# Optimization experiments

Hardware: AMD Instinct MI355X
Metric: run time of the kernel (lower is better)

Reference implementation:

```python
import jax, jax.numpy as jnp
import numpy as np

N, E, D, L, G = 100000, 800000, 64, 5, 256
ATOM_VOCAB, BOND_VOCAB = 119, 5
BN_EPS = 1e-5

def _bn(h, g, b):
    # BatchNorm1d in training mode: batch mean / biased var over nodes
    m = h.mean(0)
    v = h.var(0)
    return g * (h - m) * jax.lax.rsqrt(v + BN_EPS) + b

def setup_inputs() -> dict:
    key = jax.random.key(0)
    ks = jax.random.split(key, 12)
    xavier = lambda k, fi, fo: jax.random.uniform(k, (fi, fo), jnp.float32,
                                                  -np.sqrt(6.0/(fi+fo)), np.sqrt(6.0/(fi+fo)))
    return {
        "batch": jnp.sort(jax.random.randint(ks[0], (N,), 0, G)),
        "x": jax.random.randint(ks[1], (N, 1), 0, ATOM_VOCAB),
        "edge_index": jax.random.randint(ks[2], (2, E), 0, N),
        "edge_attr": jax.random.randint(ks[3], (E, 1), 0, BOND_VOCAB),
        "atom_emb": jax.random.normal(ks[4], (ATOM_VOCAB, D), jnp.float32),
        "bond_emb": jax.random.normal(ks[5], (BOND_VOCAB, D), jnp.float32),
        "W1": jnp.stack([xavier(jax.random.fold_in(ks[6], i), D, 2*D) for i in range(L)]),
        "b1": jnp.zeros((L, 2*D), jnp.float32),
        "g1": jnp.ones((L, 2*D), jnp.float32),
        "be1": jnp.zeros((L, 2*D), jnp.float32),
        "W2": jnp.stack([xavier(jax.random.fold_in(ks[7], i), 2*D, D) for i in range(L)]),
        "b2": jnp.zeros((L, D), jnp.float32),
        "gbn": jnp.ones((L, D), jnp.float32),
        "bbn": jnp.zeros((L, D), jnp.float32),
    }

def reference(batch, x, edge_index, edge_attr, atom_emb, bond_emb,
              W1, b1, g1, be1, W2, b2, gbn, bbn):
    h = atom_emb[x[:, 0]]              # [N, D]
    ea = bond_emb[edge_attr[:, 0]]     # [E, D]
    src, dst = edge_index[0], edge_index[1]
    for i in range(L):
        msg = jax.nn.relu(h[src] + ea)                         # [E, D]
        aggr = jax.ops.segment_sum(msg, dst, num_segments=N)   # [N, D]
        z = h + aggr                                           # (1+eps)*x_i + aggr, eps=0
        z = _bn(z @ W1[i] + b1[i], g1[i], be1[i])
        z = jax.nn.relu(z) @ W2[i] + b2[i]
        h = _bn(z, gbn[i], bbn[i])                             # outer BN
        if i < L - 1:
            h = jax.nn.relu(h)                                 # drop_ratio = 0 -> no dropout
    xpool = jax.ops.segment_sum(h, batch, num_segments=G)      # global_add_pool
    return (xpool, h)
```

## Files before the change

kernel.cpp:

```cpp
#include <hip/hip_runtime.h>
#include <cstdint>
#include <cstddef>

#define NN 100000
#define NP 100032
#define NE 800000
#define NG 256
#define NL 5
#define EPS 1e-5f
#define NSTRIPE 32

typedef __bf16 bf16x8 __attribute__((ext_vector_type(8)));
typedef float f32x4 __attribute__((ext_vector_type(4)));

__device__ __forceinline__ float bf2f(unsigned short u) {
  union { unsigned int i; float f; } x; x.i = ((unsigned int)u) << 16; return x.f;
}
__device__ __forceinline__ unsigned short f2bf(float f) {
  union { float f; unsigned int i; } x; x.f = f;
  unsigned int r = x.i + 0x7fffu + ((x.i >> 16) & 1u);
  return (unsigned short)(r >> 16);
}

__global__ __launch_bounds__(256) void prep_k(const int* __restrict__ x,
                                              const float* __restrict__ atom_emb,
                                              unsigned short* __restrict__ A,
                                              const float* __restrict__ W1,
                                              const float* __restrict__ W2,
                                              unsigned short* __restrict__ Wt1,
                                              unsigned short* __restrict__ Wt2,
                                              int* __restrict__ cnt) {
  int b = blockIdx.x, t = threadIdx.x;
  if (b < 3125) {
    int i = b * 256 + t;
    int n = i >> 3, c0 = (i & 7) * 8;
    const float* p = atom_emb + (size_t)x[n] * 64 + c0;
    float4 v0 = *(const float4*)p;
    float4 v1 = *(const float4*)(p + 4);
    union { bf16x8 b8; unsigned short u[8]; } o;
    o.u[0] = f2bf(v0.x); o.u[1] = f2bf(v0.y); o.u[2] = f2bf(v0.z); o.u[3] = f2bf(v0.w);
    o.u[4] = f2bf(v1.x); o.u[5] = f2bf(v1.y); o.u[6] = f2bf(v1.z); o.u[7] = f2bf(v1.w);
    *(bf16x8*)(A + (size_t)n * 64 + c0) = o.b8;
  } else if (b < 3445) {
    int i = (b - 3125) * 256 + t;
    const int S = NL * 128 * 64;
    if (i < S) {
      int l = i / (128 * 64), r = i % (128 * 64);
      int c = r / 64, k = r % 64;
      Wt1[i] = f2bf(W1[(size_t)l * 64 * 128 + (size_t)k * 128 + c]);
    } else {
      int j = i - S;
      int l = j / (128 * 64), r = j % (128 * 64);
      int c = r / 128, k = r % 128;
      Wt2[j] = f2bf(W2[(size_t)l * 128 * 64 + (size_t)k * 64 + c]);
    }
  } else {
    int i = (b - 3445) * 256 + t;
    if (i < NN) cnt[i] = 0;
  }
}

__global__ __launch_bounds__(256) void hist_k(const int* __restrict__ ei,
                                              int* __restrict__ cnt) {
  int e = blockIdx.x * 256 + threadIdx.x;
  if (e >= NE) return;
  atomicAdd(&cnt[ei[NE + e]], 1);
}

__global__ __launch_bounds__(256) void scan1_k(const int* __restrict__ cnt,
                                               int* __restrict__ rs,
                                               int* __restrict__ bsum) {
  __shared__ int sh[256];
  int t = threadIdx.x;
  int base = blockIdx.x * 1024 + t * 4;
  int v0 = 0, v1 = 0, v2 = 0, v3 = 0;
  if (base + 0 < NN) v0 = cnt[base + 0];
  if (base + 1 < NN) v1 = cnt[base + 1];
  if (base + 2 < NN) v2 = cnt[base + 2];
  if (base + 3 < NN) v3 = cnt[base + 3];
  int tsum = v0 + v1 + v2 + v3;
  sh[t] = tsum;
  __syncthreads();
  for (int off = 1; off < 256; off <<= 1) {
    int x = (t >= off) ? sh[t - off] : 0;
    __syncthreads();
    sh[t] += x;
    __syncthreads();
  }
  int excl = sh[t] - tsum;
  if (base + 0 < NN) rs[base + 0] = excl;
  if (base + 1 < NN) rs[base + 1] = excl + v0;
  if (base + 2 < NN) rs[base + 2] = excl + v0 + v1;
  if (base + 3 < NN) rs[base + 3] = excl + v0 + v1 + v2;
  if (t == 255) bsum[blockIdx.x] = sh[255];
}

__global__ __launch_bounds__(256) void scan3_k(int* __restrict__ rs,
                                               const int* __restrict__ bsum,
                                               int* __restrict__ cursor) {
  int i = blockIdx.x * 256 + threadIdx.x;
  int chunk = blockIdx.x >> 2;
  int boff = 0;
  for (int j = 0; j < chunk; ++j) boff += bsum[j];
  if (i < NN) {
    int v = rs[i] + boff;
    rs[i] = v;
    cursor[i] = v;
  }
  if (i == 0) rs[NN] = NE;
}

__global__ __launch_bounds__(256) void scatter_k(const int* __restrict__ ei,
                                                 const int* __restrict__ eattr,
                                                 int* __restrict__ cursor,
                                                 int* __restrict__ epack) {
  int band = blockIdx.x & 7;
  int e = (blockIdx.x >> 3) * 256 + threadIdx.x;
  if (e >= NE) return;
  int d = ei[NE + e];
  if (d / 12500 != band) return;
  int slot = atomicAdd(&cursor[d], 1);
  epack[slot] = (ei[e] << 3) | eattr[e];
}

template <int MODE>
__global__ __launch_bounds__(256) void csr_aggr_k(const int* __restrict__ rowstart,
                                                  const int* __restrict__ epack,
                                                  const float* __restrict__ bond,
                                                  const unsigned short* __restrict__ A,
                                                  const float* __restrict__ stat2prev,
                                                  const float* __restrict__ g,
                                                  const float* __restrict__ be,
                                                  unsigned short* __restrict__ B) {
  __shared__ float bl[5][68];
  __shared__ float scl64[64], shf64[64];
  int tid = threadIdx.x;
  for (int j = tid; j < 320; j += 256) bl[j >> 6][j & 63] = bond[j];
  if (MODE && tid < 64) {
    float s = 0.f, s2 = 0.f;
#pragma unroll
    for (int r = 0; r < NSTRIPE; ++r) {
      s += stat2prev[r * 128 + tid];
      s2 += stat2prev[r * 128 + 64 + tid];
    }
    float mean = s * (1.f / NN);
    float var = fmaxf(s2 * (1.f / NN) - mean * mean, 0.f);
    float sc = g[tid] * rsqrtf(var + EPS);
    scl64[tid] = sc;
    shf64[tid] = be[tid] - mean * sc;
  }
  __syncthreads();

  int lane = tid & 63;
  int sg = lane >> 3, ch = lane & 7, c0 = ch * 8;
  int row = blockIdx.x * 32 + (tid >> 6) * 8 + sg;
  float sc[8], sf[8];
  if (MODE) {
#pragma unroll
    for (int j = 0; j < 8; ++j) { sc[j] = scl64[c0 + j]; sf[j] = shf64[c0 + j]; }
  }
  int s = rowstart[row], e = rowstart[row + 1];
  float acc[8];
#pragma unroll
  for (int j = 0; j < 8; ++j) acc[j] = 0.f;
  int i = s;
  for (; i + 2 <= e; i += 2) {
    int p0 = epack[i], p1 = epack[i + 1];
    union { bf16x8 b; unsigned short u[8]; } h0, h1;
    h0.b = *(const bf16x8*)(A + (size_t)(p0 >> 3) * 64 + c0);
    h1.b = *(const bf16x8*)(A + (size_t)(p1 >> 3) * 64 + c0);
    const float* bp0 = &bl[p0 & 7][c0];
    const float* bp1 = &bl[p1 & 7][c0];
    float4 a0 = *(const float4*)(bp0), a1 = *(const float4*)(bp0 + 4);
    float4 d0 = *(const float4*)(bp1), d1 = *(const float4*)(bp1 + 4);
    float bb0[8] = {a0.x, a0.y, a0.z, a0.w, a1.x, a1.y, a1.z, a1.w};
    float bb1[8] = {d0.x, d0.y, d0.z, d0.w, d1.x, d1.y, d1.z, d1.w};
#pragma unroll
    for (int j = 0; j < 8; ++j) {
      float v0 = bf2f(h0.u[j]);
      float v1 = bf2f(h1.u[j]);
      if (MODE) {
        v0 = fmaxf(fmaf(v0, sc[j], sf[j]), 0.f);
        v1 = fmaxf(fmaf(v1, sc[j], sf[j]), 0.f);
      }
      acc[j] += fmaxf(v0 + bb0[j], 0.f);
      acc[j] += fmaxf(v1 + bb1[j], 0.f);
    }
  }
  if (i < e) {
    int p0 = epack[i];
    union { bf16x8 b; unsigned short u[8]; } h0;
    h0.b = *(const bf16x8*)(A + (size_t)(p0 >> 3) * 64 + c0);
    const float* bp0 = &bl[p0 & 7][c0];
    float4 a0 = *(const float4*)(bp0), a1 = *(const float4*)(bp0 + 4);
    float bb0[8] = {a0.x, a0.y, a0.z, a0.w, a1.x, a1.y, a1.z, a1.w};
#pragma unroll
    for (int j = 0; j < 8; ++j) {
      float v0 = bf2f(h0.u[j]);
      if (MODE) v0 = fmaxf(fmaf(v0, sc[j], sf[j]), 0.f);
      acc[j] += fmaxf(v0 + bb0[j], 0.f);
    }
  }
  union { bf16x8 b; unsigned short u[8]; } rv, o;
  rv.b = *(const bf16x8*)(A + (size_t)row * 64 + c0);
#pragma unroll
  for (int j = 0; j < 8; ++j) {
    float r = bf2f(rv.u[j]);
    if (MODE) r = fmaxf(fmaf(r, sc[j], sf[j]), 0.f);
    o.u[j] = f2bf(acc[j] + r);
  }
  *(bf16x8*)(B + (size_t)row * 64 + c0) = o.b;
}

__global__ __launch_bounds__(256) void stat1_k(const unsigned short* __restrict__ B,
                                               const unsigned short* __restrict__ Wt1,
                                               float* __restrict__ stat1) {
  int tid = threadIdx.x;
  int w = tid >> 6, lane = tid & 63;
  int rlo = lane & 15, khi = lane >> 4;
  int t = blockIdx.x * 4 + w;
  union { bf16x8 b; uint4 u; } zz; zz.u = make_uint4(0, 0, 0, 0);
  bf16x8 a0 = zz.b, a1 = zz.b;
  if (t < NP / 16) {
    int row = t * 16 + rlo;
    if (row < NN) {
      const bf16x8* ap = (const bf16x8*)(B + (size_t)row * 64 + khi * 8);
      a0 = ap[0]; a1 = ap[4];
    }
  }
  float s[8], s2[8];
#pragma unroll
  for (int ct = 0; ct < 8; ++ct) { s[ct] = 0.f; s2[ct] = 0.f; }
  if (t < NP / 16) {
#pragma unroll
    for (int ct = 0; ct < 8; ++ct) {
      const bf16x8* bp = (const bf16x8*)(Wt1 + (size_t)(ct * 16 + rlo) * 64 + khi * 8);
      f32x4 acc;
      acc[0] = 0.f; acc[1] = 0.f; acc[2] = 0.f; acc[3] = 0.f;
      acc = __builtin_amdgcn_mfma_f32_16x16x32_bf16(a0, bp[0], acc, 0, 0, 0);
      acc = __builtin_amdgcn_mfma_f32_16x16x32_bf16(a1, bp[4], acc, 0, 0, 0);
#pragma unroll
      for (int q = 0; q < 4; ++q) {
        s[ct] += acc[q];
        s2[ct] = fmaf(acc[q], acc[q], s2[ct]);
      }
    }
  }
#pragma unroll
  for (int ct = 0; ct < 8; ++ct) {
    s[ct] += __shfl_xor(s[ct], 16);  s[ct] += __shfl_xor(s[ct], 32);
    s2[ct] += __shfl_xor(s2[ct], 16); s2[ct] += __shfl_xor(s2[ct], 32);
  }
  if (khi == 0 && t < NP / 16) {
    float* dst = stat1 + (blockIdx.x & (NSTRIPE - 1)) * 256;
#pragma unroll
    for (int ct = 0; ct < 8; ++ct) {
      atomicAdd(&dst[ct * 16 + rlo], s[ct]);
      atomicAdd(&dst[128 + ct * 16 + rlo], s2[ct]);
    }
  }
}

__global__ __launch_bounds__(256) void gemm12_k(const unsigned short* __restrict__ B,
                                                const unsigned short* __restrict__ Wt1,
                                                const unsigned short* __restrict__ Wt2,
                                                const float* __restrict__ stat1,
                                                const float* __restrict__ g1,
                                                const float* __restrict__ be1,
                                                const float* __restrict__ b2,
                                                unsigned short* __restrict__ z2b,
                                                float* __restrict__ stat2f) {
  __shared__ unsigned short Zs[64][136];
  __shared__ float sclS[128], shfS[128], sred[128];
  int tid = threadIdx.x;
  int w = tid >> 6, lane = tid & 63;
  int rlo = lane & 15, khi = lane >> 4;
  int row0 = blockIdx.x * 64 + w * 16;
  const bf16x8* ap = (const bf16x8*)(B + (size_t)(row0 + rlo) * 64 + khi * 8);
  bf16x8 a0 = ap[0], a1 = ap[4];
  if (tid < 128) {
    float s = 0.f, s2 = 0.f;
#pragma unroll
    for (int r = 0; r < NSTRIPE; ++r) {
      s += stat1[r * 256 + tid];
      s2 += stat1[r * 256 + 128 + tid];
    }
    float mean = s * (1.f / NN);
    float var = fmaxf(s2 * (1.f / NN) - mean * mean, 0.f);
    float sc = g1[tid] * rsqrtf(var + EPS);
    sclS[tid] = sc;
    shfS[tid] = be1[tid] - mean * sc;
    sred[tid] = 0.f;
  }
  __syncthreads();
#pragma unroll
  for (int ct = 0; ct < 8; ++ct) {
    const bf16x8* bp = (const bf16x8*)(Wt1 + (size_t)(ct * 16 + rlo) * 64 + khi * 8);
    f32x4 acc;
    acc[0] = 0.f; acc[1] = 0.f; acc[2] = 0.f; acc[3] = 0.f;
    acc = __builtin_amdgcn_mfma_f32_16x16x32_bf16(a0, bp[0], acc, 0, 0, 0);
    acc = __builtin_amdgcn_mfma_f32_16x16x32_bf16(a1, bp[4], acc, 0, 0, 0);
    int c = ct * 16 + rlo;
    float sc = sclS[c], sf = shfS[c];
#pragma unroll
    for (int q = 0; q < 4; ++q)
      Zs[w * 16 + khi * 4 + q][c] = f2bf(fmaxf(fmaf(acc[q], sc, sf), 0.f));
  }
  bf16x8 af0 = *(const bf16x8*)&Zs[w * 16 + rlo][khi * 8];
  bf16x8 af1 = *(const bf16x8*)&Zs[w * 16 + rlo][32 + khi * 8];
  bf16x8 af2 = *(const bf16x8*)&Zs[w * 16 + rlo][64 + khi * 8];
  bf16x8 af3 = *(const bf16x8*)&Zs[w * 16 + rlo][96 + khi * 8];
  __syncthreads();
  f32x4 acc2[4];
#pragma unroll
  for (int ct = 0; ct < 4; ++ct) { acc2[ct][0] = 0.f; acc2[ct][1] = 0.f; acc2[ct][2] = 0.f; acc2[ct][3] = 0.f; }
#pragma unroll
  for (int ct = 0; ct < 4; ++ct) {
    const bf16x8* bp = (const bf16x8*)(Wt2 + (size_t)(ct * 16 + rlo) * 128 + khi * 8);
    acc2[ct] = __builtin_amdgcn_mfma_f32_16x16x32_bf16(af0, bp[0], acc2[ct], 0, 0, 0);
    acc2[ct] = __builtin_amdgcn_mfma_f32_16x16x32_bf16(af1, bp[4], acc2[ct], 0, 0, 0);
    acc2[ct] = __builtin_amdgcn_mfma_f32_16x16x32_bf16(af2, bp[8], acc2[ct], 0, 0, 0);
    acc2[ct] = __builtin_amdgcn_mfma_f32_16x16x32_bf16(af3, bp[12], acc2[ct], 0, 0, 0);
  }
  unsigned short (*Z2)[72] = (unsigned short(*)[72])Zs;
#pragma unroll
  for (int ct = 0; ct < 4; ++ct) {
    int c = ct * 16 + rlo;
    float bs = b2[c];
    float s = 0.f, s2 = 0.f;
#pragma unroll
    for (int q = 0; q < 4; ++q) {
      int brow = w * 16 + khi * 4 + q;
      float v = acc2[ct][q] + bs;
      unsigned short ub = f2bf(v);
      Z2[brow][c] = ub;
      float vf = bf2f(ub);
      if (blockIdx.x * 64 + brow < NN) { s += vf; s2 += vf * vf; }
    }
    s += __shfl_xor(s, 16);  s += __shfl_xor(s, 32);
    s2 += __shfl_xor(s2, 16); s2 += __shfl_xor(s2, 32);
    if (khi == 0) {
      atomicAdd(&sred[c], s);
      atomicAdd(&sred[64 + c], s2);
    }
  }
  __syncthreads();
#pragma unroll
  for (int pass = 0; pass < 2; ++pass) {
    int orow = pass * 32 + (tid >> 3), oc0 = (tid & 7) * 8;
    *(bf16x8*)(z2b + (size_t)(blockIdx.x * 64 + orow) * 64 + oc0) =
        *(const bf16x8*)&Z2[orow][oc0];
  }
  if (tid < 128)
    atomicAdd(&stat2f[(blockIdx.x & (NSTRIPE - 1)) * 128 + tid], sred[tid]);
}

__global__ __launch_bounds__(256) void final_k(const unsigned short* __restrict__ A,
                                               const float* __restrict__ stat2f,
                                               const float* __restrict__ g,
                                               const float* __restrict__ be,
                                               const int* __restrict__ batch,
                                               float* __restrict__ hf,
                                               float* __restrict__ xpool) {
  __shared__ float scl[64], shf[64];
  __shared__ float red[16][64];
  __shared__ int gfirst, gsame;
  int tid = threadIdx.x;
  if (tid < 64) {
    float s = 0.f, s2 = 0.f;
#pragma unroll
    for (int r = 0; r < NSTRIPE; ++r) {
      s += stat2f[r * 128 + tid];
      s2 += stat2f[r * 128 + 64 + tid];
    }
    float mean = s * (1.f / NN);
    float var = fmaxf(s2 * (1.f / NN) - mean * mean, 0.f);
    float sc = g[tid] * rsqrtf(var + EPS);
    scl[tid] = sc;
    shf[tid] = be[tid] - mean * sc;
  }
  int n0 = blockIdx.x * 16;
  if (tid == 0) {
    gfirst = batch[n0];
    gsame = (batch[n0] == batch[n0 + 15]) ? 1 : 0;
  }
  __syncthreads();
  int r = tid >> 4, c4 = tid & 15;
  int n = n0 + r;
  ushort4 raw = *(const ushort4*)(A + (size_t)n * 64 + c4 * 4);
  int cb = c4 * 4;
  float4 v;
  v.x = fmaf(bf2f(raw.x), scl[cb + 0], shf[cb + 0]);
  v.y = fmaf(bf2f(raw.y), scl[cb + 1], shf[cb + 1]);
  v.z = fmaf(bf2f(raw.z), scl[cb + 2], shf[cb + 2]);
  v.w = fmaf(bf2f(raw.w), scl[cb + 3], shf[cb + 3]);
  *(float4*)(hf + (size_t)n * 64 + cb) = v;
  *(float4*)&red[r][cb] = v;
  __syncthreads();
  if (gsame) {
#pragma unroll
    for (int off = 8; off >= 1; off >>= 1) {
      if (r < off) {
        float4 a = *(float4*)&red[r][cb];
        float4 b = *(float4*)&red[r + off][cb];
        *(float4*)&red[r][cb] = make_float4(a.x + b.x, a.y + b.y, a.z + b.z, a.w + b.w);
      }
      __syncthreads();
    }
    if (r == 0) {
      float* p = xpool + (size_t)gfirst * 64 + cb;
      float4 a = *(float4*)&red[0][cb];
      atomicAdd(p + 0, a.x); atomicAdd(p + 1, a.y);
      atomicAdd(p + 2, a.z); atomicAdd(p + 3, a.w);
    }
  } else {
    int gg = batch[n];
    float* p = xpool + (size_t)gg * 64 + cb;
    atomicAdd(p + 0, v.x); atomicAdd(p + 1, v.y);
    atomicAdd(p + 2, v.z); atomicAdd(p + 3, v.w);
  }
}

extern "C" void kernel_launch(void* const* d_in, const int* in_sizes, int n_in,
                              void* d_out, int out_size, void* d_ws, size_t ws_size,
                              hipStream_t stream) {
  const int* batch = (const int*)d_in[0];
  const int* x = (const int*)d_in[1];
  const int* ei = (const int*)d_in[2];
  const int* eattr = (const int*)d_in[3];
  const float* atom_emb = (const float*)d_in[4];
  const float* bond_emb = (const float*)d_in[5];
  const float* W1 = (const float*)d_in[6];
  const float* g1 = (const float*)d_in[8];
  const float* be1 = (const float*)d_in[9];
  const float* W2 = (const float*)d_in[10];
  const float* b2 = (const float*)d_in[11];
  const float* gbn = (const float*)d_in[12];
  const float* bbn = (const float*)d_in[13];

  float* out = (float*)d_out;
  float* xpool = out;
  float* hf = out + NG * 64;

  char* ws = (char*)d_ws;
  unsigned short* A   = (unsigned short*)(ws);
  unsigned short* B   = (unsigned short*)(ws + 12804096);
  float* sbuf         = (float*)(ws + 25608192);
  unsigned short* Wt1 = (unsigned short*)(ws + 25853952);
  unsigned short* Wt2 = (unsigned short*)(ws + 25935872);
  int* rowstart       = (int*)(ws + 26017792);
  int* epack          = (int*)(ws + 26417796);
  int* cnt    = (int*)(ws + 12804096);
  int* cursor = (int*)(ws + 12804096 + 1048576);
  int* bsum   = (int*)(ws + 12804096 + 2097152);

  prep_k<<<3836, 256, 0, stream>>>(x, atom_emb, A, W1, W2, Wt1, Wt2, cnt);

  hist_k<<<(NE + 255) / 256, 256, 0, stream>>>(ei, cnt);
  scan1_k<<<98, 256, 0, stream>>>(cnt, rowstart, bsum);
  scan3_k<<<(NN + 255) / 256, 256, 0, stream>>>(rowstart, bsum, cursor);
  scatter_k<<<8 * ((NE + 255) / 256), 256, 0, stream>>>(ei, eattr, cursor, epack);

  hipMemsetAsync(sbuf, 0, 245760, stream);
  for (int l = 0; l < NL; ++l) {
    float* stat1 = sbuf + (size_t)l * 12288;
    float* stat2 = sbuf + (size_t)l * 12288 + 8192;
    float* stat2p = sbuf + (size_t)(l - 1) * 12288 + 8192;
    if (l == 0)
      csr_aggr_k<0><<<NN / 32, 256, 0, stream>>>(rowstart, epack, bond_emb, A,
                                                 sbuf, gbn, bbn, B);
    else
      csr_aggr_k<1><<<NN / 32, 256, 0, stream>>>(rowstart, epack, bond_emb, A,
                                                 stat2p, gbn + (size_t)(l - 1) * 64,
                                                 bbn + (size_t)(l - 1) * 64, B);
    stat1_k<<<(NP / 16 + 3) / 4, 256, 0, stream>>>(B, Wt1 + (size_t)l * 128 * 64, stat1);
    gemm12_k<<<NP / 64, 256, 0, stream>>>(B, Wt1 + (size_t)l * 128 * 64,
                                          Wt2 + (size_t)l * 64 * 128,
                                          stat1, g1 + (size_t)l * 128, be1 + (size_t)l * 128,
                                          b2 + (size_t)l * 64, A, stat2);
  }

  hipMemsetAsync(xpool, 0, (size_t)NG * 64 * 4, stream);
  final_k<<<NN / 16, 256, 0, stream>>>(A, sbuf + (size_t)(NL - 1) * 12288 + 8192,
                                       gbn + (size_t)(NL - 1) * 64,
                                       bbn + (size_t)(NL - 1) * 64, batch, hf, xpool);
}
```

Before: 530.2 us.

## Fuse first-BN statistics GEMM into CSR aggregation kernel; halve scatter bands

The stat1 kernel, which recomputed B@W1 only to gather BatchNorm sums, is folded into the aggregation kernel. Each block stages its 32 output rows in shared memory and runs MFMA on them to accumulate per-column sums and sums of squares with atomics. This saves one launch per layer and a full re-read of B, at the cost of an extra barrier and more work in the gather kernel. The scatter kernel's destination banding also drops from 8 bands to 4, which means fewer redundant passes over the edge list but less locality in the atomic cursor updates.

```diff
diff --git a/kernel.cpp b/kernel.cpp
--- a/kernel.cpp
+++ b/kernel.cpp
@@ -114,11 +114,11 @@
                                                  const int* __restrict__ eattr,
                                                  int* __restrict__ cursor,
                                                  int* __restrict__ epack) {
-  int band = blockIdx.x & 7;
-  int e = (blockIdx.x >> 3) * 256 + threadIdx.x;
+  int band = blockIdx.x & 3;
+  int e = (blockIdx.x >> 2) * 256 + threadIdx.x;
   if (e >= NE) return;
   int d = ei[NE + e];
-  if (d / 12500 != band) return;
+  if (d / 25000 != band) return;
   int slot = atomicAdd(&cursor[d], 1);
   epack[slot] = (ei[e] << 3) | eattr[e];
 }
@@ -131,9 +131,12 @@
                                                   const float* __restrict__ stat2prev,
                                                   const float* __restrict__ g,
                                                   const float* __restrict__ be,
-                                                  unsigned short* __restrict__ B) {
+                                                  const unsigned short* __restrict__ Wt1,
+                                                  unsigned short* __restrict__ B,
+                                                  float* __restrict__ stat1) {
   __shared__ float bl[5][68];
   __shared__ float scl64[64], shf64[64];
+  __shared__ unsigned short Bs[32][72];
   int tid = threadIdx.x;
   for (int j = tid; j < 320; j += 256) bl[j >> 6][j & 63] = bond[j];
   if (MODE && tid < 64) {
@@ -153,7 +156,8 @@
 
   int lane = tid & 63;
   int sg = lane >> 3, ch = lane & 7, c0 = ch * 8;
-  int row = blockIdx.x * 32 + (tid >> 6) * 8 + sg;
+  int rloc = (tid >> 6) * 8 + sg;
+  int row = blockIdx.x * 32 + rloc;
   float sc[8], sf[8];
   if (MODE) {
 #pragma unroll
@@ -210,53 +214,34 @@
     o.u[j] = f2bf(acc[j] + r);
   }
   *(bf16x8*)(B + (size_t)row * 64 + c0) = o.b;
-}
-
-__global__ __launch_bounds__(256) void stat1_k(const unsigned short* __restrict__ B,
-                                               const unsigned short* __restrict__ Wt1,
-                                               float* __restrict__ stat1) {
-  int tid = threadIdx.x;
-  int w = tid >> 6, lane = tid & 63;
+  *(bf16x8*)&Bs[rloc][c0] = o.b;
+  __syncthreads();
+
+  int w = tid >> 6;
   int rlo = lane & 15, khi = lane >> 4;
-  int t = blockIdx.x * 4 + w;
-  union { bf16x8 b; uint4 u; } zz; zz.u = make_uint4(0, 0, 0, 0);
-  bf16x8 a0 = zz.b, a1 = zz.b;
-  if (t < NP / 16) {
-    int row = t * 16 + rlo;
-    if (row < NN) {
-      const bf16x8* ap = (const bf16x8*)(B + (size_t)row * 64 + khi * 8);
-      a0 = ap[0]; a1 = ap[4];
-    }
-  }
-  float s[8], s2[8];
-#pragma unroll
-  for (int ct = 0; ct < 8; ++ct) { s[ct] = 0.f; s2[ct] = 0.f; }
-  if (t < NP / 16) {
-#pragma unroll
-    for (int ct = 0; ct < 8; ++ct) {
-      const bf16x8* bp = (const bf16x8*)(Wt1 + (size_t)(ct * 16 + rlo) * 64 + khi * 8);
-      f32x4 acc;
-      acc[0] = 0.f; acc[1] = 0.f; acc[2] = 0.f; acc[3] = 0.f;
-      acc = __builtin_amdgcn_mfma_f32_16x16x32_bf16(a0, bp[0], acc, 0, 0, 0);
-      acc = __builtin_amdgcn_mfma_f32_16x16x32_bf16(a1, bp[4], acc, 0, 0, 0);
-#pragma unroll
-      for (int q = 0; q < 4; ++q) {
-        s[ct] += acc[q];
-        s2[ct] = fmaf(acc[q], acc[q], s2[ct]);
-      }
-    }
-  }
-#pragma unroll
-  for (int ct = 0; ct < 8; ++ct) {
-    s[ct] += __shfl_xor(s[ct], 16);  s[ct] += __shfl_xor(s[ct], 32);
-    s2[ct] += __shfl_xor(s2[ct], 16); s2[ct] += __shfl_xor(s2[ct], 32);
-  }
-  if (khi == 0 && t < NP / 16) {
-    float* dst = stat1 + (blockIdx.x & (NSTRIPE - 1)) * 256;
-#pragma unroll
-    for (int ct = 0; ct < 8; ++ct) {
-      atomicAdd(&dst[ct * 16 + rlo], s[ct]);
-      atomicAdd(&dst[128 + ct * 16 + rlo], s2[ct]);
+  int tile = w >> 1, gcol = (w & 1) * 64;
+  bf16x8 fa0 = *(const bf16x8*)&Bs[tile * 16 + rlo][khi * 8];
+  bf16x8 fa1 = *(const bf16x8*)&Bs[tile * 16 + rlo][khi * 8 + 32];
+  float* dst = stat1 + (blockIdx.x & (NSTRIPE - 1)) * 256;
+#pragma unroll
+  for (int ct = 0; ct < 4; ++ct) {
+    int c = gcol + ct * 16 + rlo;
+    const bf16x8* bp = (const bf16x8*)(Wt1 + (size_t)c * 64 + khi * 8);
+    f32x4 yacc;
+    yacc[0] = 0.f; yacc[1] = 0.f; yacc[2] = 0.f; yacc[3] = 0.f;
+    yacc = __builtin_amdgcn_mfma_f32_16x16x32_bf16(fa0, bp[0], yacc, 0, 0, 0);
+    yacc = __builtin_amdgcn_mfma_f32_16x16x32_bf16(fa1, bp[4], yacc, 0, 0, 0);
+    float ss = 0.f, ss2 = 0.f;
+#pragma unroll
+    for (int q = 0; q < 4; ++q) {
+      ss += yacc[q];
+      ss2 = fmaf(yacc[q], yacc[q], ss2);
+    }
+    ss += __shfl_xor(ss, 16);  ss += __shfl_xor(ss, 32);
+    ss2 += __shfl_xor(ss2, 16); ss2 += __shfl_xor(ss2, 32);
+    if (khi == 0) {
+      atomicAdd(&dst[c], ss);
+      atomicAdd(&dst[128 + c], ss2);
     }
   }
 }
@@ -459,7 +444,7 @@
   hist_k<<<(NE + 255) / 256, 256, 0, stream>>>(ei, cnt);
   scan1_k<<<98, 256, 0, stream>>>(cnt, rowstart, bsum);
   scan3_k<<<(NN + 255) / 256, 256, 0, stream>>>(rowstart, bsum, cursor);
-  scatter_k<<<8 * ((NE + 255) / 256), 256, 0, stream>>>(ei, eattr, cursor, epack);
+  scatter_k<<<4 * ((NE + 255) / 256), 256, 0, stream>>>(ei, eattr, cursor, epack);
 
   hipMemsetAsync(sbuf, 0, 245760, stream);
   for (int l = 0; l < NL; ++l) {
@@ -468,12 +453,13 @@
     float* stat2p = sbuf + (size_t)(l - 1) * 12288 + 8192;
     if (l == 0)
       csr_aggr_k<0><<<NN / 32, 256, 0, stream>>>(rowstart, epack, bond_emb, A,
-                                                 sbuf, gbn, bbn, B);
+                                                 sbuf, gbn, bbn,
+                                                 Wt1, B, stat1);
     else
       csr_aggr_k<1><<<NN / 32, 256, 0, stream>>>(rowstart, epack, bond_emb, A,
                                                  stat2p, gbn + (size_t)(l - 1) * 64,
-                                                 bbn + (size_t)(l - 1) * 64, B);
-    stat1_k<<<(NP / 16 + 3) / 4, 256, 0, stream>>>(B, Wt1 + (size_t)l * 128 * 64, stat1);
+                                                 bbn + (size_t)(l - 1) * 64,
+                                                 Wt1 + (size_t)l * 128 * 64, B, stat1);
     gemm12_k<<<NP / 64, 256, 0, stream>>>(B, Wt1 + (size_t)l * 128 * 64,
                                           Wt2 + (size_t)l * 64 * 128,
                                           stat1, g1 + (size_t)l * 128, be1 + (size_t)l * 128,
```

After: 484.8 us. 8.6% less time.
